# Kernel optimization log

Measured on AMD Instinct MI355X. Metric: run time of the kernel, lower is better.

## Reference

```python
import jax, jax.numpy as jnp
import numpy as np

N, E, D, H, C, G, L = 100000, 1600000, 128, 4, 32, 4096, 3  # nodes, edges, h_dim, heads, head_dim, graphs, conv blocks


def setup_inputs() -> dict:
    key = jax.random.key(0)
    ks = jax.random.split(key, 24)
    s = 0.05
    w = lambda k, shape: jax.random.normal(k, shape, jnp.float32) * s
    inp = {
        "x": jax.random.normal(ks[0], (N, D), jnp.float32),
        "edge_index": jax.random.randint(ks[1], (2, E), 0, N),
        "batch": jnp.sort(jax.random.randint(ks[2], (N,), 0, G)),
        # input TransformerConv (in=D, out=C per head, H heads, beta=True)
        "in_Wq": w(ks[3], (D, D)), "in_bq": jnp.zeros((D,), jnp.float32),
        "in_Wk": w(ks[4], (D, D)), "in_bk": jnp.zeros((D,), jnp.float32),
        "in_Wv": w(ks[5], (D, D)), "in_bv": jnp.zeros((D,), jnp.float32),
        "in_Ws": w(ks[6], (D, D)), "in_bs": jnp.zeros((D,), jnp.float32),
        "in_Wbeta": w(ks[7], (3 * D,)),
        # stacked conv blocks (L of them, in=out=D)
        "blk_Wq": w(ks[8], (L, D, D)), "blk_bq": jnp.zeros((L, D), jnp.float32),
        "blk_Wk": w(ks[9], (L, D, D)), "blk_bk": jnp.zeros((L, D), jnp.float32),
        "blk_Wv": w(ks[10], (L, D, D)), "blk_bv": jnp.zeros((L, D), jnp.float32),
        "blk_Ws": w(ks[11], (L, D, D)), "blk_bs": jnp.zeros((L, D), jnp.float32),
        "blk_Wbeta": w(ks[12], (L, 3 * D)),
        # MLP head
        "W1": w(ks[13], (D, 64)), "b1": jnp.zeros((64,), jnp.float32),
        "W2": w(ks[14], (64, 32)), "b2": jnp.zeros((32,), jnp.float32),
        "W3": w(ks[15], (32, 1)), "b3": jnp.zeros((1,), jnp.float32),
    }
    return inp


def transformer_conv(x, src, dst, Wq, bq, Wk, bk, Wv, bv, Ws, bs, Wbeta):
    # PyG TransformerConv, concat=True, root_weight=True, beta=True, eval mode
    q = (x @ Wq + bq).reshape(N, H, C)
    k = (x @ Wk + bk).reshape(N, H, C)
    v = (x @ Wv + bv).reshape(N, H, C)
    # per-edge attention logits: message j=src -> i=dst
    alpha = jnp.einsum("ehc,ehc->eh", q[dst], k[src]) / jnp.sqrt(jnp.float32(C))  # [E,H]
    m = jax.ops.segment_max(alpha, dst, num_segments=N)
    m = jnp.where(jnp.isfinite(m), m, 0.0)
    e = jnp.exp(alpha - m[dst])
    denom = jax.ops.segment_sum(e, dst, num_segments=N)
    a = e / (denom[dst] + 1e-16)  # segment softmax over in-edges of dst
    msg = a[..., None] * v[src]  # [E,H,C]
    out = jax.ops.segment_sum(msg, dst, num_segments=N).reshape(N, H * C)
    x_r = x @ Ws + bs
    beta = jax.nn.sigmoid(jnp.concatenate([out, x_r, out - x_r], axis=-1) @ Wbeta)[:, None]
    return beta * x_r + (1.0 - beta) * out


def reference(x, edge_index, batch, in_Wq, in_bq, in_Wk, in_bk, in_Wv, in_bv,
              in_Ws, in_bs, in_Wbeta, blk_Wq, blk_bq, blk_Wk, blk_bk, blk_Wv,
              blk_bv, blk_Ws, blk_bs, blk_Wbeta, W1, b1, W2, b2, W3, b3):
    src, dst = edge_index[0], edge_index[1]
    h = jax.nn.relu(transformer_conv(x, src, dst, in_Wq, in_bq, in_Wk, in_bk,
                                     in_Wv, in_bv, in_Ws, in_bs, in_Wbeta))
    for l in range(L):  # dropout is identity in eval mode
        h = jax.nn.relu(transformer_conv(h, src, dst, blk_Wq[l], blk_bq[l],
                                         blk_Wk[l], blk_bk[l], blk_Wv[l], blk_bv[l],
                                         blk_Ws[l], blk_bs[l], blk_Wbeta[l]))
    # global mean pool over graphs
    sums = jax.ops.segment_sum(h, batch, num_segments=G)
    cnt = jax.ops.segment_sum(jnp.ones((N, 1), h.dtype), batch, num_segments=G)
    g = sums / jnp.maximum(cnt, 1.0)
    g = jax.nn.relu(g @ W1 + b1)
    g = jax.nn.relu(g @ W2 + b2)
    return jax.nn.sigmoid(g @ W3 + b3)
```

## Files before the change

kernel.cpp:

```cpp
#include <hip/hip_runtime.h>
#include <hip/hip_bf16.h>
#include <cstdint>

#define DH 128
#define NB 256
#define NBK 1024

typedef __attribute__((ext_vector_type(8))) short short8;
typedef __attribute__((ext_vector_type(4))) float floatx4;
typedef __attribute__((ext_vector_type(2))) float floatx2;

__device__ __forceinline__ float bflo(unsigned u) { return __uint_as_float(u << 16); }
__device__ __forceinline__ float bfhi(unsigned u) { return __uint_as_float(u & 0xffff0000u); }

__device__ __forceinline__ unsigned pk_bf16(float a, float b) {
  return ((unsigned)__bfloat16_as_ushort(__float2bfloat16(b)) << 16)
       | (unsigned)__bfloat16_as_ushort(__float2bfloat16(a));
}

template<int CTRL>
__device__ __forceinline__ float dpp_add(float x) {
  int y = __builtin_amdgcn_update_dpp(0, __float_as_int(x), CTRL, 0xf, 0xf, true);
  return x + __int_as_float(y);
}


__global__ __launch_bounds__(256)
void csr_p1(const int* __restrict__ dst, int* __restrict__ hist, int E, int chunk) {
  __shared__ int cnt[NBK];
  const int blk = blockIdx.x, tid = threadIdx.x;
  for (int c = tid; c < NBK; c += 256) cnt[c] = 0;
  __syncthreads();
  int base = blk * chunk;
  int end = base + chunk; if (end > E) end = E;
  for (int e = base + tid; e < end; e += 256) atomicAdd(&cnt[dst[e] >> 7], 1);
  __syncthreads();
  for (int c = tid; c < NBK; c += 256) hist[c * NB + blk] = cnt[c];
}

__global__ __launch_bounds__(256)
void csr_p2(int* __restrict__ hist, int* __restrict__ total) {
  int b = blockIdx.x * 4 + (threadIdx.x >> 6);
  int lane = threadIdx.x & 63;
  int4 v = *(int4*)&hist[b * NB + lane * 4];
  int s0 = v.x;
  int s1 = s0 + v.y;
  int s2 = s1 + v.z;
  int s3 = s2 + v.w;
  int t = s3;
  for (int d = 1; d < 64; d <<= 1) {
    int y = __shfl_up(t, d);
    if (lane >= d) t += y;
  }
  int excl = t - s3;
  int4 o;
  o.x = excl; o.y = excl + s0; o.z = excl + s1; o.w = excl + s2;
  *(int4*)&hist[b * NB + lane * 4] = o;
  if (lane == 63) total[b] = t;
}

__global__ __launch_bounds__(1024)
void scan_tstart(const int* __restrict__ total, int* __restrict__ tstart) {
  __shared__ int sh[1024];
  int t = threadIdx.x;
  int v = total[t];
  sh[t] = v;
  __syncthreads();
  for (int d = 1; d < 1024; d <<= 1) {
    int x = (t >= d) ? sh[t - d] : 0;
    __syncthreads();
    sh[t] += x;
    __syncthreads();
  }
  tstart[t] = sh[t] - v;
}

__global__ __launch_bounds__(256)
void csr_p3(const int* __restrict__ src, const int* __restrict__ dst,
            const int* __restrict__ hist, const int* __restrict__ tstart,
            int* __restrict__ part, int E, int chunk) {
  __shared__ int cur[NBK];
  const int blk = blockIdx.x, tid = threadIdx.x;
  for (int c = tid; c < NBK; c += 256) cur[c] = hist[c * NB + blk] + tstart[c];
  __syncthreads();
  int base = blk * chunk;
  int end = base + chunk; if (end > E) end = E;
  for (int e = base + tid; e < end; e += 256) {
    int d = dst[e];
    int b = d >> 7;
    int pos = atomicAdd(&cur[b], 1);
    part[pos] = (src[e] << 7) | (d & 127);
  }
}

__global__ __launch_bounds__(256)
void csr_p4(const int* __restrict__ part, const int* __restrict__ tstart,
            const int* __restrict__ total, int* __restrict__ deg,
            int* __restrict__ off, int* __restrict__ csr, int Nn) {
  __shared__ int lcnt[128], lscan[128], lcur[128];
  const int b = blockIdx.x, tid = threadIdx.x;
  const int p0 = tstart[b];
  const int m = total[b];
  if (tid < 128) lcnt[tid] = 0;
  __syncthreads();
  for (int k = tid; k < m; k += 256) atomicAdd(&lcnt[part[p0 + k] & 127], 1);
  __syncthreads();
  if (tid < 128) lscan[tid] = lcnt[tid];
  __syncthreads();
  for (int d = 1; d < 128; d <<= 1) {
    int v = 0;
    if (tid < 128 && tid >= d) v = lscan[tid - d];
    __syncthreads();
    if (tid < 128) lscan[tid] += v;
    __syncthreads();
  }
  if (tid < 128) {
    int ex = lscan[tid] - lcnt[tid];
    lcur[tid] = ex;
    int n = (b << 7) + tid;
    if (n < Nn) { deg[n] = lcnt[tid]; off[n] = p0 + ex; }
  }
  __syncthreads();
  for (int k = tid; k < m; k += 256) {
    int pk = part[p0 + k];
    int pos = p0 + atomicAdd(&lcur[pk & 127], 1);
    csr[pos] = pk >> 7;
  }
}


__global__ void goff_kernel(const int* __restrict__ batch, int* __restrict__ goff,
                            int N, int G) {
  int g = blockIdx.x * 256 + threadIdx.x;
  if (g > G) return;
  if (g == G) { goff[G] = N; return; }
  int lo = 0, hi = N;
  while (lo < hi) { int mid = (lo + hi) >> 1; if (batch[mid] < g) lo = mid + 1; else hi = mid; }
  goff[g] = lo;
}


__global__ __launch_bounds__(256)
void pack_w_kernel(const float* __restrict__ iWq, const float* __restrict__ iWk,
                   const float* __restrict__ iWv, const float* __restrict__ iWs,
                   const float* __restrict__ ibq, const float* __restrict__ ibk,
                   const float* __restrict__ ibv, const float* __restrict__ ibs,
                   const float* __restrict__ bWq, const float* __restrict__ bWk,
                   const float* __restrict__ bWv, const float* __restrict__ bWs,
                   const float* __restrict__ bbq, const float* __restrict__ bbk,
                   const float* __restrict__ bbv, const float* __restrict__ bbs,
                   __hip_bfloat16* __restrict__ WT2, float* __restrict__ bcat) {
  const int layer = blockIdx.x / 65;
  const int bid = blockIdx.x % 65;
  const float *Wq, *Wk, *Wv, *Ws, *bq, *bk, *bv, *bs;
  if (layer == 0) {
    Wq = iWq; Wk = iWk; Wv = iWv; Ws = iWs; bq = ibq; bk = ibk; bv = ibv; bs = ibs;
  } else {
    int m = layer - 1;
    Wq = bWq + (size_t)m * DH * DH; Wk = bWk + (size_t)m * DH * DH;
    Wv = bWv + (size_t)m * DH * DH; Ws = bWs + (size_t)m * DH * DH;
    bq = bbq + (size_t)m * DH; bk = bbk + (size_t)m * DH;
    bv = bbv + (size_t)m * DH; bs = bbs + (size_t)m * DH;
  }
  unsigned short* WT2l = (unsigned short*)WT2 + (size_t)layer * 65536;
  float* bcl = bcat + layer * 512;

  if (bid == 64) {
    for (int c = threadIdx.x; c < 512; c += 256) {
      int which = c >> 7, cc = c & 127;
      const float* b = (which == 0) ? bq : (which == 1) ? bk : (which == 2) ? bv : bs;
      bcl[c] = b[cc];
    }
    return;
  }
  __shared__ float tile[32][33];
  const int which = bid >> 4, kb = (bid >> 2) & 3, cb = bid & 3;
  const float* W = (which == 0) ? Wq : (which == 1) ? Wk : (which == 2) ? Wv : Ws;
  const int tx = threadIdx.x & 31, ty = threadIdx.x >> 5;
#pragma unroll
  for (int r = ty; r < 32; r += 8)
    tile[r][tx] = W[(kb * 32 + r) * 128 + cb * 32 + tx];
  __syncthreads();
  const int t = threadIdx.x;
  const int mt_sel = t >> 7;
  const int s4 = (t & 127) * 4;
  const int l16 = s4 >> 5;
  const int quad = (s4 >> 3) & 3;
  const int j0 = s4 & 7;
  const int cl = mt_sel * 16 + l16;
  const int kr = quad * 8 + j0;
  float f0 = tile[kr + 0][cl];
  float f1 = tile[kr + 1][cl];
  float f2 = tile[kr + 2][cl];
  float f3 = tile[kr + 3][cl];
  const int mt = which * 8 + cb * 2 + mt_sel;
  const int o = mt * 2048 + kb * 512 + l16 * 32 + quad * 8 + j0;
  uint2 w;
  w.x = pk_bf16(f0, f1);
  w.y = pk_bf16(f2, f3);
  *(uint2*)&WT2l[o] = w;
}


template<int F32IN>
__global__ __launch_bounds__(256)
void gemm_qkvs(const void* __restrict__ Xin, const short* __restrict__ WT2,
               const float* __restrict__ bc,
               unsigned int* __restrict__ qout,
               unsigned int* __restrict__ kvp,
               unsigned int* __restrict__ xrout, int Nn) {
  __shared__ short As[32][132];
  const int row0 = blockIdx.x * 32;
  const int tid = threadIdx.x;

#pragma unroll
  for (int p = 0; p < 2; ++p) {
    int chunk = p * 256 + tid;
    int r = chunk >> 4, c8 = chunk & 15;
    int row = row0 + r; if (row >= Nn) row = Nn - 1;
    if (F32IN) {
      const float* xf = (const float*)Xin + (size_t)row * 128 + c8 * 8;
      float4 f0 = *(const float4*)xf;
      float4 f1 = *(const float4*)(xf + 4);
      int4 pk;
      ((unsigned*)&pk)[0] = pk_bf16(f0.x, f0.y);
      ((unsigned*)&pk)[1] = pk_bf16(f0.z, f0.w);
      ((unsigned*)&pk)[2] = pk_bf16(f1.x, f1.y);
      ((unsigned*)&pk)[3] = pk_bf16(f1.z, f1.w);
      *(int4*)&As[r][c8 * 8] = pk;
    } else {
      *(int4*)&As[r][c8 * 8] = *(const int4*)((const short*)Xin + (size_t)row * 128 + c8 * 8);
    }
  }
  __syncthreads();

  const int w = tid >> 6, lane = tid & 63, quad = lane >> 4, l16 = lane & 15;

  short8 xf[2][4];
#pragma unroll
  for (int nt = 0; nt < 2; ++nt)
#pragma unroll
    for (int kt = 0; kt < 4; ++kt)
      xf[nt][kt] = *(const short8*)&As[nt * 16 + l16][kt * 32 + quad * 8];

  const int fbase = l16 * 32 + quad * 8;

  if (w == 0 || w == 3) {
    unsigned int* outp = (w == 0) ? qout : xrout;
    const int mbase = (w == 0) ? 0 : 24;
#pragma unroll
    for (int i = 0; i < 8; ++i) {
      const int mt = mbase + i;
      short8 af[4];
#pragma unroll
      for (int kt = 0; kt < 4; ++kt)
        af[kt] = *(const short8*)&WT2[mt * 2048 + kt * 512 + fbase];
      float4 bias = *(const float4*)&bc[mt * 16 + quad * 4];
      const int wc = (i * 16 + quad * 4);
#pragma unroll
      for (int nt = 0; nt < 2; ++nt) {
        floatx4 acc = (floatx4){0.f, 0.f, 0.f, 0.f};
#pragma unroll
        for (int kt = 0; kt < 4; ++kt)
          acc = __builtin_amdgcn_mfma_f32_16x16x32_bf16(af[kt], xf[nt][kt], acc, 0, 0, 0);
        int node = row0 + nt * 16 + l16;
        if (node < Nn) {
          uint2 o;
          o.x = pk_bf16(acc[0] + bias.x, acc[1] + bias.y);
          o.y = pk_bf16(acc[2] + bias.z, acc[3] + bias.w);
          *(uint2*)&outp[(size_t)node * 64 + (wc >> 1)] = o;
        }
      }
    }
  } else {
    const int kb = 8 + (w - 1) * 4;
    const int vb = 16 + (w - 1) * 4;
#pragma unroll
    for (int i = 0; i < 4; ++i) {
      const int mk = kb + i, mv = vb + i;
      short8 afk[4], afv[4];
#pragma unroll
      for (int kt = 0; kt < 4; ++kt) {
        afk[kt] = *(const short8*)&WT2[mk * 2048 + kt * 512 + fbase];
        afv[kt] = *(const short8*)&WT2[mv * 2048 + kt * 512 + fbase];
      }
      float4 bk4 = *(const float4*)&bc[mk * 16 + quad * 4];
      float4 bv4 = *(const float4*)&bc[mv * 16 + quad * 4];
      const int krel = (w - 1) * 64 + i * 16 + quad * 4;
#pragma unroll
      for (int nt = 0; nt < 2; ++nt) {
        floatx4 ak = (floatx4){0.f, 0.f, 0.f, 0.f};
        floatx4 av = (floatx4){0.f, 0.f, 0.f, 0.f};
#pragma unroll
        for (int kt = 0; kt < 4; ++kt) {
          ak = __builtin_amdgcn_mfma_f32_16x16x32_bf16(afk[kt], xf[nt][kt], ak, 0, 0, 0);
          av = __builtin_amdgcn_mfma_f32_16x16x32_bf16(afv[kt], xf[nt][kt], av, 0, 0, 0);
        }
        int node = row0 + nt * 16 + l16;
        if (node < Nn) {
          int d0 = __builtin_amdgcn_cvt_pk_fp8_f32(ak[0] + bk4.x, ak[1] + bk4.y, 0, false);
          d0 = __builtin_amdgcn_cvt_pk_fp8_f32(av[0] + bv4.x, av[1] + bv4.y, d0, true);
          int d1 = __builtin_amdgcn_cvt_pk_fp8_f32(ak[2] + bk4.z, ak[3] + bk4.w, 0, false);
          d1 = __builtin_amdgcn_cvt_pk_fp8_f32(av[2] + bv4.z, av[3] + bv4.w, d1, true);
          uint2 o; o.x = (unsigned)d0; o.y = (unsigned)d1;
          *(uint2*)&kvp[(size_t)node * 64 + (krel >> 1)] = o;
        }
      }
    }
  }
}


__global__ __launch_bounds__(256)
void attn_kernel(unsigned int* __restrict__ q_h, const uint4* __restrict__ kvq,
                 const uint4* __restrict__ xr4, const int* __restrict__ off,
                 const int* __restrict__ deg, const int* __restrict__ csr,
                 const float* __restrict__ Wb, int Nn) {
  int wv = __builtin_amdgcn_readfirstlane(threadIdx.x >> 6);
  int i = blockIdx.x * 4 + wv;
  if (i >= Nn) return;
  const int l = threadIdx.x & 63;
  const int j = l & 15;
  const int g = l >> 4;

  const float QS = 0.17677669529663687f * 1.4426950408889634f;
  uint4 qw = ((const uint4*)q_h)[(size_t)i * 16 + j];
  float q0 = bflo(qw.x) * QS, q1 = bfhi(qw.x) * QS;
  float q2 = bflo(qw.y) * QS, q3 = bfhi(qw.y) * QS;
  float q4 = bflo(qw.z) * QS, q5 = bfhi(qw.z) * QS;
  float q6 = bflo(qw.w) * QS, q7 = bfhi(qw.w) * QS;

  const int e0 = off[i];
  const int dg = deg[i];
  const int eend = e0 + dg;

  float denA = 0.f, denB = 0.f;
  float aA[8] = {0.f, 0.f, 0.f, 0.f, 0.f, 0.f, 0.f, 0.f};
  float aB[8] = {0.f, 0.f, 0.f, 0.f, 0.f, 0.f, 0.f, 0.f};

  auto comp = [&](const uint4& kv, bool valid, float& den, float (&a)[8]) {
    floatx2 k0 = __builtin_amdgcn_cvt_pk_f32_fp8((int)kv.x, false);
    floatx2 v0 = __builtin_amdgcn_cvt_pk_f32_fp8((int)kv.x, true);
    floatx2 k1 = __builtin_amdgcn_cvt_pk_f32_fp8((int)kv.y, false);
    floatx2 v1 = __builtin_amdgcn_cvt_pk_f32_fp8((int)kv.y, true);
    floatx2 k2 = __builtin_amdgcn_cvt_pk_f32_fp8((int)kv.z, false);
    floatx2 v2 = __builtin_amdgcn_cvt_pk_f32_fp8((int)kv.z, true);
    floatx2 k3 = __builtin_amdgcn_cvt_pk_f32_fp8((int)kv.w, false);
    floatx2 v3 = __builtin_amdgcn_cvt_pk_f32_fp8((int)kv.w, true);
    float d = q0 * k0.x + q1 * k0.y + q2 * k1.x + q3 * k1.y
            + q4 * k2.x + q5 * k2.y + q6 * k3.x + q7 * k3.y;
    d = dpp_add<0xB1>(d);
    d = dpp_add<0x4E>(d);
    float p = valid ? exp2f(d) : 0.f;
    den += p;
    a[0] += p * v0.x; a[1] += p * v0.y; a[2] += p * v1.x; a[3] += p * v1.y;
    a[4] += p * v2.x; a[5] += p * v2.y; a[6] += p * v3.x; a[7] += p * v3.y;
  };

  for (int e = e0; e < eend; e += 64) {
    const int rem = eend - e;
    const int take = (rem < 64) ? rem : 64;
    int il = e + l; if (il >= eend) il = eend - 1;
    const int sv = csr[il];

    for (int b = 0; b < take; b += 16) {
      uint4 kv0, kv1, kv2, kv3;
      bool p0 = false, p1 = false, p2 = false, p3 = false;
      const int c0 = b + g, c1 = b + 4 + g, c2 = b + 8 + g, c3 = b + 12 + g;
      {
        p0 = c0 < take;
        int s = __shfl(sv, p0 ? c0 : 0);
        kv0 = kvq[(unsigned)((s << 4) | j)];
      }
      if (b + 4 < take) {
        p1 = c1 < take;
        int s = __shfl(sv, p1 ? c1 : 0);
        kv1 = kvq[(unsigned)((s << 4) | j)];
      }
      if (b + 8 < take) {
        p2 = c2 < take;
        int s = __shfl(sv, p2 ? c2 : 0);
        kv2 = kvq[(unsigned)((s << 4) | j)];
      }
      if (b + 12 < take) {
        p3 = c3 < take;
        int s = __shfl(sv, p3 ? c3 : 0);
        kv3 = kvq[(unsigned)((s << 4) | j)];
      }
      comp(kv0, p0, denA, aA);
      if (b + 4 < take)  comp(kv1, p1, denB, aB);
      if (b + 8 < take)  comp(kv2, p2, denA, aA);
      if (b + 12 < take) comp(kv3, p3, denB, aB);
    }
  }

  uint4 xw = xr4[(size_t)i * 16 + j];
  float4 wo0 = *(const float4*)&Wb[8 * j];
  float4 wo1 = *(const float4*)&Wb[8 * j + 4];
  float4 wx0 = *(const float4*)&Wb[128 + 8 * j];
  float4 wx1 = *(const float4*)&Wb[128 + 8 * j + 4];
  float4 wd0 = *(const float4*)&Wb[256 + 8 * j];
  float4 wd1 = *(const float4*)&Wb[256 + 8 * j + 4];

  float den = denA + denB;
  float a0 = aA[0] + aB[0], a1 = aA[1] + aB[1], a2 = aA[2] + aB[2], a3 = aA[3] + aB[3];
  float a4 = aA[4] + aB[4], a5 = aA[5] + aB[5], a6 = aA[6] + aB[6], a7 = aA[7] + aB[7];

  den += __shfl_xor(den, 16); den += __shfl_xor(den, 32);
  a0 += __shfl_xor(a0, 16); a0 += __shfl_xor(a0, 32);
  a1 += __shfl_xor(a1, 16); a1 += __shfl_xor(a1, 32);
  a2 += __shfl_xor(a2, 16); a2 += __shfl_xor(a2, 32);
  a3 += __shfl_xor(a3, 16); a3 += __shfl_xor(a3, 32);
  a4 += __shfl_xor(a4, 16); a4 += __shfl_xor(a4, 32);
  a5 += __shfl_xor(a5, 16); a5 += __shfl_xor(a5, 32);
  a6 += __shfl_xor(a6, 16); a6 += __shfl_xor(a6, 32);
  a7 += __shfl_xor(a7, 16); a7 += __shfl_xor(a7, 32);

  float inv = 1.f / (den + 1e-16f);
  float o0 = a0 * inv, o1 = a1 * inv, o2 = a2 * inv, o3 = a3 * inv;
  float o4 = a4 * inv, o5 = a5 * inv, o6 = a6 * inv, o7 = a7 * inv;

  float x0 = bflo(xw.x), x1 = bfhi(xw.x);
  float x2 = bflo(xw.y), x3 = bfhi(xw.y);
  float x4 = bflo(xw.z), x5 = bfhi(xw.z);
  float x6 = bflo(xw.w), x7 = bfhi(xw.w);

  float c = o0 * wo0.x + o1 * wo0.y + o2 * wo0.z + o3 * wo0.w
          + o4 * wo1.x + o5 * wo1.y + o6 * wo1.z + o7 * wo1.w
          + x0 * wx0.x + x1 * wx0.y + x2 * wx0.z + x3 * wx0.w
          + x4 * wx1.x + x5 * wx1.y + x6 * wx1.z + x7 * wx1.w
          + (o0 - x0) * wd0.x + (o1 - x1) * wd0.y + (o2 - x2) * wd0.z + (o3 - x3) * wd0.w
          + (o4 - x4) * wd1.x + (o5 - x5) * wd1.y + (o6 - x6) * wd1.z + (o7 - x7) * wd1.w;
  c = dpp_add<0xB1>(c);
  c = dpp_add<0x4E>(c);
  c = dpp_add<0x141>(c);
  c = dpp_add<0x140>(c);
  float beta = 1.f / (1.f + __expf(-c));

  if (g == 0) {
    float h0 = fmaxf(beta * x0 + (1.f - beta) * o0, 0.f);
    float h1 = fmaxf(beta * x1 + (1.f - beta) * o1, 0.f);
    float h2 = fmaxf(beta * x2 + (1.f - beta) * o2, 0.f);
    float h3 = fmaxf(beta * x3 + (1.f - beta) * o3, 0.f);
    float h4 = fmaxf(beta * x4 + (1.f - beta) * o4, 0.f);
    float h5 = fmaxf(beta * x5 + (1.f - beta) * o5, 0.f);
    float h6 = fmaxf(beta * x6 + (1.f - beta) * o6, 0.f);
    float h7 = fmaxf(beta * x7 + (1.f - beta) * o7, 0.f);
    uint4 hw;
    hw.x = pk_bf16(h0, h1);
    hw.y = pk_bf16(h2, h3);
    hw.z = pk_bf16(h4, h5);
    hw.w = pk_bf16(h6, h7);
    ((uint4*)q_h)[(size_t)i * 16 + j] = hw;
  }
}


__global__ __launch_bounds__(128)
void poolmlp_kernel(const unsigned short* __restrict__ h, const int* __restrict__ goff,
                    const float* __restrict__ W1, const float* __restrict__ b1,
                    const float* __restrict__ W2, const float* __restrict__ b2,
                    const float* __restrict__ W3, const float* __restrict__ b3,
                    float* __restrict__ out) {
  int g = blockIdx.x;
  int t = threadIdx.x;
  int n0 = goff[g], cnt = goff[g + 1] - n0;
  float s = 0.f;
  for (int n = n0; n < n0 + cnt; ++n) s += bflo(h[(size_t)n * 128 + t]);
  __shared__ float gv[128];
  __shared__ float t1[64];
  __shared__ float t2[32];
  gv[t] = s / fmaxf((float)cnt, 1.0f);
  __syncthreads();
  if (t < 64) {
    float a = b1[t];
    for (int k = 0; k < 128; ++k) a += gv[k] * W1[k * 64 + t];
    t1[t] = fmaxf(a, 0.f);
  }
  __syncthreads();
  if (t < 32) {
    float a = b2[t];
    for (int k = 0; k < 64; ++k) a += t1[k] * W2[k * 32 + t];
    t2[t] = fmaxf(a, 0.f);
  }
  __syncthreads();
  if (t == 0) {
    float a = b3[0];
    for (int k = 0; k < 32; ++k) a += t2[k] * W3[k];
    out[g] = 1.f / (1.f + __expf(-a));
  }
}


extern "C" void kernel_launch(void* const* d_in, const int* in_sizes, int n_in,
                              void* d_out, int out_size, void* d_ws, size_t ws_size,
                              hipStream_t stream) {
  const float* x = (const float*)d_in[0];
  const int* edge_index = (const int*)d_in[1];
  const int* batch = (const int*)d_in[2];
  const int N = in_sizes[0] / DH;
  const int E = in_sizes[1] / 2;
  const int G = out_size;
  const int* src = edge_index;
  const int* dst = edge_index + E;

  const float* in_Wq = (const float*)d_in[3];
  const float* in_bq = (const float*)d_in[4];
  const float* in_Wk = (const float*)d_in[5];
  const float* in_bk = (const float*)d_in[6];
  const float* in_Wv = (const float*)d_in[7];
  const float* in_bv = (const float*)d_in[8];
  const float* in_Ws = (const float*)d_in[9];
  const float* in_bs = (const float*)d_in[10];
  const float* in_Wbeta = (const float*)d_in[11];
  const float* blk_Wq = (const float*)d_in[12];
  const float* blk_bq = (const float*)d_in[13];
  const float* blk_Wk = (const float*)d_in[14];
  const float* blk_bk = (const float*)d_in[15];
  const float* blk_Wv = (const float*)d_in[16];
  const float* blk_bv = (const float*)d_in[17];
  const float* blk_Ws = (const float*)d_in[18];
  const float* blk_bs = (const float*)d_in[19];
  const float* blk_Wbeta = (const float*)d_in[20];

  char* p = (char*)d_ws;
  auto take = [&](size_t bytes) { char* r = p; p += (bytes + 255) & ~(size_t)255; return r; };
  __hip_bfloat16* h0 = (__hip_bfloat16*)take((size_t)N * DH * 2);
  __hip_bfloat16* h1 = (__hip_bfloat16*)take((size_t)N * DH * 2);
  unsigned char* kvp = (unsigned char*)take((size_t)N * 256);
  unsigned short* xr = (unsigned short*)take((size_t)N * DH * 2);
  __hip_bfloat16* WT2 = (__hip_bfloat16*)take((size_t)4 * 512 * DH * 2);
  float* bcat = (float*)take((size_t)4 * 512 * 4);
  int* deg    = (int*)take((size_t)N * 4);
  int* off    = (int*)take((size_t)N * 4);
  int* csr    = (int*)take((size_t)E * 4);
  int* part   = (int*)take((size_t)E * 4);
  int* hist   = (int*)take((size_t)NB * NBK * 4);
  int* total  = (int*)take(NBK * 4);
  int* tstart = (int*)take(NBK * 4);
  int* goff   = (int*)take((size_t)(G + 1) * 4);
  (void)n_in;
  if ((size_t)(p - (char*)d_ws) > ws_size) return;

  const int NBUCK = (N + 127) >> 7;
  const int chunk = (E + NB - 1) / NB;

  csr_p1<<<NB, 256, 0, stream>>>(dst, hist, E, chunk);
  csr_p2<<<NBK / 4, 256, 0, stream>>>(hist, total);
  scan_tstart<<<1, 1024, 0, stream>>>(total, tstart);
  csr_p3<<<NB, 256, 0, stream>>>(src, dst, hist, tstart, part, E, chunk);
  csr_p4<<<NBUCK, 256, 0, stream>>>(part, tstart, total, deg, off, csr, N);

  goff_kernel<<<(G + 256) / 256, 256, 0, stream>>>(batch, goff, N, G);

  pack_w_kernel<<<4 * 65, 256, 0, stream>>>(
      in_Wq, in_Wk, in_Wv, in_Ws, in_bq, in_bk, in_bv, in_bs,
      blk_Wq, blk_Wk, blk_Wv, blk_Ws, blk_bq, blk_bk, blk_bv, blk_bs,
      WT2, bcat);

  for (int l = 0; l < 4; ++l) {
    const float* Wb = (l == 0) ? in_Wbeta : blk_Wbeta + (size_t)(l - 1) * 3 * DH;
    const short* WT2l = (const short*)WT2 + (size_t)l * 65536;
    const float* bcl = bcat + (size_t)l * 512;
    __hip_bfloat16* hin  = (l & 1) ? h1 : h0;
    __hip_bfloat16* qbuf = (l & 1) ? h0 : h1;
    if (l == 0) {
      gemm_qkvs<1><<<(N + 31) / 32, 256, 0, stream>>>((const void*)x, WT2l, bcl,
          (unsigned int*)qbuf, (unsigned int*)kvp, (unsigned int*)xr, N);
    } else {
      gemm_qkvs<0><<<(N + 31) / 32, 256, 0, stream>>>((const void*)hin, WT2l, bcl,
          (unsigned int*)qbuf, (unsigned int*)kvp, (unsigned int*)xr, N);
    }
    attn_kernel<<<(N + 3) / 4, 256, 0, stream>>>((unsigned int*)qbuf, (const uint4*)kvp,
        (const uint4*)xr, off, deg, csr, Wb, N);
  }

  poolmlp_kernel<<<G, 128, 0, stream>>>((const unsigned short*)h0, goff,
      (const float*)d_in[21], (const float*)d_in[22],
      (const float*)d_in[23], (const float*)d_in[24],
      (const float*)d_in[25], (const float*)d_in[26],
      (float*)d_out);
}
```

Measured before the change: 678.2 us.

## Fuse CSR build, weight packing and first GEMM into fewer kernel launches

Independent preprocessing kernels (histogram pass, weight packing, graph offset search) are merged into one launch, and the CSR scatter pass is co-launched with the layer-0 QKVS GEMM in a single grid partitioned by block index. Offsets and degrees are packed into one int2 array, so attention reads one 8-byte value per node instead of two separate loads. The aim is to cut launch overhead and let independent work overlap on the GPU. In exchange, shared memory is sized for the largest branch, and the mixed-role kernels may see uneven block runtimes.

```diff
diff --git a/kernel.cpp b/kernel.cpp
--- a/kernel.cpp
+++ b/kernel.cpp
@@ -25,10 +25,8 @@
 }
 
 
-__global__ __launch_bounds__(256)
-void csr_p1(const int* __restrict__ dst, int* __restrict__ hist, int E, int chunk) {
-  __shared__ int cnt[NBK];
-  const int blk = blockIdx.x, tid = threadIdx.x;
+__device__ void csr_p1_body(int* cnt, const int* __restrict__ dst,
+                            int* __restrict__ hist, int E, int chunk, int blk, int tid) {
   for (int c = tid; c < NBK; c += 256) cnt[c] = 0;
   __syncthreads();
   int base = blk * chunk;
@@ -38,152 +36,31 @@
   for (int c = tid; c < NBK; c += 256) hist[c * NB + blk] = cnt[c];
 }
 
-__global__ __launch_bounds__(256)
-void csr_p2(int* __restrict__ hist, int* __restrict__ total) {
-  int b = blockIdx.x * 4 + (threadIdx.x >> 6);
-  int lane = threadIdx.x & 63;
-  int4 v = *(int4*)&hist[b * NB + lane * 4];
-  int s0 = v.x;
-  int s1 = s0 + v.y;
-  int s2 = s1 + v.z;
-  int s3 = s2 + v.w;
-  int t = s3;
-  for (int d = 1; d < 64; d <<= 1) {
-    int y = __shfl_up(t, d);
-    if (lane >= d) t += y;
-  }
-  int excl = t - s3;
-  int4 o;
-  o.x = excl; o.y = excl + s0; o.z = excl + s1; o.w = excl + s2;
-  *(int4*)&hist[b * NB + lane * 4] = o;
-  if (lane == 63) total[b] = t;
-}
-
-__global__ __launch_bounds__(1024)
-void scan_tstart(const int* __restrict__ total, int* __restrict__ tstart) {
-  __shared__ int sh[1024];
-  int t = threadIdx.x;
-  int v = total[t];
-  sh[t] = v;
-  __syncthreads();
-  for (int d = 1; d < 1024; d <<= 1) {
-    int x = (t >= d) ? sh[t - d] : 0;
-    __syncthreads();
-    sh[t] += x;
-    __syncthreads();
-  }
-  tstart[t] = sh[t] - v;
-}
-
-__global__ __launch_bounds__(256)
-void csr_p3(const int* __restrict__ src, const int* __restrict__ dst,
-            const int* __restrict__ hist, const int* __restrict__ tstart,
-            int* __restrict__ part, int E, int chunk) {
-  __shared__ int cur[NBK];
-  const int blk = blockIdx.x, tid = threadIdx.x;
-  for (int c = tid; c < NBK; c += 256) cur[c] = hist[c * NB + blk] + tstart[c];
-  __syncthreads();
-  int base = blk * chunk;
-  int end = base + chunk; if (end > E) end = E;
-  for (int e = base + tid; e < end; e += 256) {
-    int d = dst[e];
-    int b = d >> 7;
-    int pos = atomicAdd(&cur[b], 1);
-    part[pos] = (src[e] << 7) | (d & 127);
-  }
-}
-
-__global__ __launch_bounds__(256)
-void csr_p4(const int* __restrict__ part, const int* __restrict__ tstart,
-            const int* __restrict__ total, int* __restrict__ deg,
-            int* __restrict__ off, int* __restrict__ csr, int Nn) {
-  __shared__ int lcnt[128], lscan[128], lcur[128];
-  const int b = blockIdx.x, tid = threadIdx.x;
-  const int p0 = tstart[b];
-  const int m = total[b];
-  if (tid < 128) lcnt[tid] = 0;
-  __syncthreads();
-  for (int k = tid; k < m; k += 256) atomicAdd(&lcnt[part[p0 + k] & 127], 1);
-  __syncthreads();
-  if (tid < 128) lscan[tid] = lcnt[tid];
-  __syncthreads();
-  for (int d = 1; d < 128; d <<= 1) {
-    int v = 0;
-    if (tid < 128 && tid >= d) v = lscan[tid - d];
-    __syncthreads();
-    if (tid < 128) lscan[tid] += v;
-    __syncthreads();
-  }
-  if (tid < 128) {
-    int ex = lscan[tid] - lcnt[tid];
-    lcur[tid] = ex;
-    int n = (b << 7) + tid;
-    if (n < Nn) { deg[n] = lcnt[tid]; off[n] = p0 + ex; }
-  }
-  __syncthreads();
-  for (int k = tid; k < m; k += 256) {
-    int pk = part[p0 + k];
-    int pos = p0 + atomicAdd(&lcur[pk & 127], 1);
-    csr[pos] = pk >> 7;
-  }
-}
-
-
-__global__ void goff_kernel(const int* __restrict__ batch, int* __restrict__ goff,
-                            int N, int G) {
-  int g = blockIdx.x * 256 + threadIdx.x;
-  if (g > G) return;
-  if (g == G) { goff[G] = N; return; }
-  int lo = 0, hi = N;
-  while (lo < hi) { int mid = (lo + hi) >> 1; if (batch[mid] < g) lo = mid + 1; else hi = mid; }
-  goff[g] = lo;
-}
-
-
-__global__ __launch_bounds__(256)
-void pack_w_kernel(const float* __restrict__ iWq, const float* __restrict__ iWk,
-                   const float* __restrict__ iWv, const float* __restrict__ iWs,
-                   const float* __restrict__ ibq, const float* __restrict__ ibk,
-                   const float* __restrict__ ibv, const float* __restrict__ ibs,
-                   const float* __restrict__ bWq, const float* __restrict__ bWk,
-                   const float* __restrict__ bWv, const float* __restrict__ bWs,
-                   const float* __restrict__ bbq, const float* __restrict__ bbk,
-                   const float* __restrict__ bbv, const float* __restrict__ bbs,
-                   __hip_bfloat16* __restrict__ WT2, float* __restrict__ bcat) {
-  const int layer = blockIdx.x / 65;
-  const int bid = blockIdx.x % 65;
-  const float *Wq, *Wk, *Wv, *Ws, *bq, *bk, *bv, *bs;
-  if (layer == 0) {
-    Wq = iWq; Wk = iWk; Wv = iWv; Ws = iWs; bq = ibq; bk = ibk; bv = ibv; bs = ibs;
-  } else {
-    int m = layer - 1;
-    Wq = bWq + (size_t)m * DH * DH; Wk = bWk + (size_t)m * DH * DH;
-    Wv = bWv + (size_t)m * DH * DH; Ws = bWs + (size_t)m * DH * DH;
-    bq = bbq + (size_t)m * DH; bk = bbk + (size_t)m * DH;
-    bv = bbv + (size_t)m * DH; bs = bbs + (size_t)m * DH;
-  }
-  unsigned short* WT2l = (unsigned short*)WT2 + (size_t)layer * 65536;
-  float* bcl = bcat + layer * 512;
-
+__device__ void pack_w_body(float* tileraw,
+                            const float* __restrict__ Wq, const float* __restrict__ Wk,
+                            const float* __restrict__ Wv, const float* __restrict__ Ws,
+                            const float* __restrict__ bq, const float* __restrict__ bk,
+                            const float* __restrict__ bv, const float* __restrict__ bs,
+                            unsigned short* __restrict__ WT2l, float* __restrict__ bcl,
+                            int bid, int tid) {
   if (bid == 64) {
-    for (int c = threadIdx.x; c < 512; c += 256) {
+    for (int c = tid; c < 512; c += 256) {
       int which = c >> 7, cc = c & 127;
       const float* b = (which == 0) ? bq : (which == 1) ? bk : (which == 2) ? bv : bs;
       bcl[c] = b[cc];
     }
     return;
   }
-  __shared__ float tile[32][33];
+  float (*tile)[33] = (float(*)[33])tileraw;
   const int which = bid >> 4, kb = (bid >> 2) & 3, cb = bid & 3;
   const float* W = (which == 0) ? Wq : (which == 1) ? Wk : (which == 2) ? Wv : Ws;
-  const int tx = threadIdx.x & 31, ty = threadIdx.x >> 5;
+  const int tx = tid & 31, ty = tid >> 5;
 #pragma unroll
   for (int r = ty; r < 32; r += 8)
     tile[r][tx] = W[(kb * 32 + r) * 128 + cb * 32 + tx];
   __syncthreads();
-  const int t = threadIdx.x;
-  const int mt_sel = t >> 7;
-  const int s4 = (t & 127) * 4;
+  const int mt_sel = tid >> 7;
+  const int s4 = (tid & 127) * 4;
   const int l16 = s4 >> 5;
   const int quad = (s4 >> 3) & 3;
   const int j0 = s4 & 7;
@@ -201,18 +78,11 @@
   *(uint2*)&WT2l[o] = w;
 }
 
-
 template<int F32IN>
-__global__ __launch_bounds__(256)
-void gemm_qkvs(const void* __restrict__ Xin, const short* __restrict__ WT2,
-               const float* __restrict__ bc,
-               unsigned int* __restrict__ qout,
-               unsigned int* __restrict__ kvp,
-               unsigned int* __restrict__ xrout, int Nn) {
-  __shared__ short As[32][132];
-  const int row0 = blockIdx.x * 32;
-  const int tid = threadIdx.x;
-
+__device__ void gemm_body(short (*As)[132], const void* __restrict__ Xin,
+                          const short* __restrict__ WT2, const float* __restrict__ bc,
+                          unsigned int* __restrict__ qout, unsigned int* __restrict__ kvp,
+                          unsigned int* __restrict__ xrout, int Nn, int row0, int tid) {
 #pragma unroll
   for (int p = 0; p < 2; ++p) {
     int chunk = p * 256 + tid;
@@ -310,12 +180,168 @@
   }
 }
 
+__device__ void csr_p3_body(int* cur, const int* __restrict__ src, const int* __restrict__ dst,
+                            const int* __restrict__ hist, const int* __restrict__ tstart,
+                            int* __restrict__ part, int E, int chunk, int blk, int tid) {
+  for (int c = tid; c < NBK; c += 256) cur[c] = hist[c * NB + blk] + tstart[c];
+  __syncthreads();
+  int base = blk * chunk;
+  int end = base + chunk; if (end > E) end = E;
+  for (int e = base + tid; e < end; e += 256) {
+    int d = dst[e];
+    int b = d >> 7;
+    int pos = atomicAdd(&cur[b], 1);
+    part[pos] = (src[e] << 7) | (d & 127);
+  }
+}
+
+
+__global__ __launch_bounds__(256)
+void fused_pre(const int* __restrict__ dst, int* __restrict__ hist, int E, int chunk,
+               const int* __restrict__ batch, int* __restrict__ goff, int N, int G,
+               const float* __restrict__ iWq, const float* __restrict__ iWk,
+               const float* __restrict__ iWv, const float* __restrict__ iWs,
+               const float* __restrict__ ibq, const float* __restrict__ ibk,
+               const float* __restrict__ ibv, const float* __restrict__ ibs,
+               const float* __restrict__ bWq, const float* __restrict__ bWk,
+               const float* __restrict__ bWv, const float* __restrict__ bWs,
+               const float* __restrict__ bbq, const float* __restrict__ bbk,
+               const float* __restrict__ bbv, const float* __restrict__ bbs,
+               __hip_bfloat16* __restrict__ WT2, float* __restrict__ bcat) {
+  __shared__ int smem[1056];
+  const int bid = blockIdx.x, tid = threadIdx.x;
+  if (bid < NB) {
+    csr_p1_body(smem, dst, hist, E, chunk, bid, tid);
+  } else if (bid < NB + 260) {
+    const int pb = bid - NB;
+    const int layer = pb / 65, sub = pb % 65;
+    const float *Wq, *Wk, *Wv, *Ws, *bq, *bk, *bv, *bs;
+    if (layer == 0) {
+      Wq = iWq; Wk = iWk; Wv = iWv; Ws = iWs; bq = ibq; bk = ibk; bv = ibv; bs = ibs;
+    } else {
+      int m = layer - 1;
+      Wq = bWq + (size_t)m * DH * DH; Wk = bWk + (size_t)m * DH * DH;
+      Wv = bWv + (size_t)m * DH * DH; Ws = bWs + (size_t)m * DH * DH;
+      bq = bbq + (size_t)m * DH; bk = bbk + (size_t)m * DH;
+      bv = bbv + (size_t)m * DH; bs = bbs + (size_t)m * DH;
+    }
+    pack_w_body((float*)smem, Wq, Wk, Wv, Ws, bq, bk, bv, bs,
+                (unsigned short*)WT2 + (size_t)layer * 65536, bcat + layer * 512, sub, tid);
+  } else {
+    int g = (bid - NB - 260) * 256 + tid;
+    if (g > G) return;
+    if (g == G) { goff[G] = N; return; }
+    int lo = 0, hi = N;
+    while (lo < hi) { int mid = (lo + hi) >> 1; if (batch[mid] < g) lo = mid + 1; else hi = mid; }
+    goff[g] = lo;
+  }
+}
+
+__global__ __launch_bounds__(256)
+void csr_p2(int* __restrict__ hist, int* __restrict__ total) {
+  int b = blockIdx.x * 4 + (threadIdx.x >> 6);
+  int lane = threadIdx.x & 63;
+  int4 v = *(int4*)&hist[b * NB + lane * 4];
+  int s0 = v.x;
+  int s1 = s0 + v.y;
+  int s2 = s1 + v.z;
+  int s3 = s2 + v.w;
+  int t = s3;
+  for (int d = 1; d < 64; d <<= 1) {
+    int y = __shfl_up(t, d);
+    if (lane >= d) t += y;
+  }
+  int excl = t - s3;
+  int4 o;
+  o.x = excl; o.y = excl + s0; o.z = excl + s1; o.w = excl + s2;
+  *(int4*)&hist[b * NB + lane * 4] = o;
+  if (lane == 63) total[b] = t;
+}
+
+__global__ __launch_bounds__(1024)
+void scan_tstart(const int* __restrict__ total, int* __restrict__ tstart) {
+  __shared__ int sh[1024];
+  int t = threadIdx.x;
+  int v = total[t];
+  sh[t] = v;
+  __syncthreads();
+  for (int d = 1; d < 1024; d <<= 1) {
+    int x = (t >= d) ? sh[t - d] : 0;
+    __syncthreads();
+    sh[t] += x;
+    __syncthreads();
+  }
+  tstart[t] = sh[t] - v;
+}
+
+__global__ __launch_bounds__(256)
+void fused_g0p3(const void* __restrict__ Xin, const short* __restrict__ WT2,
+                const float* __restrict__ bc,
+                unsigned int* __restrict__ qout, unsigned int* __restrict__ kvp,
+                unsigned int* __restrict__ xrout, int Nn,
+                const int* __restrict__ src, const int* __restrict__ dst,
+                const int* __restrict__ hist, const int* __restrict__ tstart,
+                int* __restrict__ part, int E, int chunk) {
+  __shared__ int4 smem4[528];
+  const int tid = threadIdx.x;
+  if (blockIdx.x < NB) {
+    csr_p3_body((int*)smem4, src, dst, hist, tstart, part, E, chunk, blockIdx.x, tid);
+  } else {
+    gemm_body<1>((short(*)[132])smem4, Xin, WT2, bc, qout, kvp, xrout, Nn,
+                 (blockIdx.x - NB) * 32, tid);
+  }
+}
+
+__global__ __launch_bounds__(256)
+void csr_p4(const int* __restrict__ part, const int* __restrict__ tstart,
+            const int* __restrict__ total, int2* __restrict__ offdeg,
+            int* __restrict__ csr, int Nn) {
+  __shared__ int lcnt[128], lscan[128], lcur[128];
+  const int b = blockIdx.x, tid = threadIdx.x;
+  const int p0 = tstart[b];
+  const int m = total[b];
+  if (tid < 128) lcnt[tid] = 0;
+  __syncthreads();
+  for (int k = tid; k < m; k += 256) atomicAdd(&lcnt[part[p0 + k] & 127], 1);
+  __syncthreads();
+  if (tid < 128) lscan[tid] = lcnt[tid];
+  __syncthreads();
+  for (int d = 1; d < 128; d <<= 1) {
+    int v = 0;
+    if (tid < 128 && tid >= d) v = lscan[tid - d];
+    __syncthreads();
+    if (tid < 128) lscan[tid] += v;
+    __syncthreads();
+  }
+  if (tid < 128) {
+    int ex = lscan[tid] - lcnt[tid];
+    lcur[tid] = ex;
+    int n = (b << 7) + tid;
+    if (n < Nn) offdeg[n] = make_int2(p0 + ex, lcnt[tid]);
+  }
+  __syncthreads();
+  for (int k = tid; k < m; k += 256) {
+    int pk = part[p0 + k];
+    int pos = p0 + atomicAdd(&lcur[pk & 127], 1);
+    csr[pos] = pk >> 7;
+  }
+}
+
+__global__ __launch_bounds__(256)
+void gemm_qkvs(const short* __restrict__ Xin, const short* __restrict__ WT2,
+               const float* __restrict__ bc,
+               unsigned int* __restrict__ qout, unsigned int* __restrict__ kvp,
+               unsigned int* __restrict__ xrout, int Nn) {
+  __shared__ int4 smem4[528];
+  gemm_body<0>((short(*)[132])smem4, (const void*)Xin, WT2, bc, qout, kvp, xrout, Nn,
+               blockIdx.x * 32, threadIdx.x);
+}
+
 
 __global__ __launch_bounds__(256)
 void attn_kernel(unsigned int* __restrict__ q_h, const uint4* __restrict__ kvq,
-                 const uint4* __restrict__ xr4, const int* __restrict__ off,
-                 const int* __restrict__ deg, const int* __restrict__ csr,
-                 const float* __restrict__ Wb, int Nn) {
+                 const uint4* __restrict__ xr4, const int2* __restrict__ offdeg,
+                 const int* __restrict__ csr, const float* __restrict__ Wb, int Nn) {
   int wv = __builtin_amdgcn_readfirstlane(threadIdx.x >> 6);
   int i = blockIdx.x * 4 + wv;
   if (i >= Nn) return;
@@ -325,13 +351,14 @@
 
   const float QS = 0.17677669529663687f * 1.4426950408889634f;
   uint4 qw = ((const uint4*)q_h)[(size_t)i * 16 + j];
+  int2 od = offdeg[i];
   float q0 = bflo(qw.x) * QS, q1 = bfhi(qw.x) * QS;
   float q2 = bflo(qw.y) * QS, q3 = bfhi(qw.y) * QS;
   float q4 = bflo(qw.z) * QS, q5 = bfhi(qw.z) * QS;
   float q6 = bflo(qw.w) * QS, q7 = bfhi(qw.w) * QS;
 
-  const int e0 = off[i];
-  const int dg = deg[i];
+  const int e0 = od.x;
+  const int dg = od.y;
   const int eend = e0 + dg;
 
   float denA = 0.f, denB = 0.f;
@@ -531,8 +558,7 @@
   unsigned short* xr = (unsigned short*)take((size_t)N * DH * 2);
   __hip_bfloat16* WT2 = (__hip_bfloat16*)take((size_t)4 * 512 * DH * 2);
   float* bcat = (float*)take((size_t)4 * 512 * 4);
-  int* deg    = (int*)take((size_t)N * 4);
-  int* off    = (int*)take((size_t)N * 4);
+  int2* offdeg = (int2*)take((size_t)N * 8);
   int* csr    = (int*)take((size_t)E * 4);
   int* part   = (int*)take((size_t)E * 4);
   int* hist   = (int*)take((size_t)NB * NBK * 4);
@@ -544,35 +570,37 @@
 
   const int NBUCK = (N + 127) >> 7;
   const int chunk = (E + NB - 1) / NB;
-
-  csr_p1<<<NB, 256, 0, stream>>>(dst, hist, E, chunk);
-  csr_p2<<<NBK / 4, 256, 0, stream>>>(hist, total);
-  scan_tstart<<<1, 1024, 0, stream>>>(total, tstart);
-  csr_p3<<<NB, 256, 0, stream>>>(src, dst, hist, tstart, part, E, chunk);
-  csr_p4<<<NBUCK, 256, 0, stream>>>(part, tstart, total, deg, off, csr, N);
-
-  goff_kernel<<<(G + 256) / 256, 256, 0, stream>>>(batch, goff, N, G);
-
-  pack_w_kernel<<<4 * 65, 256, 0, stream>>>(
+  const int gblocks = (G + 256) / 256;
+
+  fused_pre<<<NB + 260 + gblocks, 256, 0, stream>>>(
+      dst, hist, E, chunk, batch, goff, N, G,
       in_Wq, in_Wk, in_Wv, in_Ws, in_bq, in_bk, in_bv, in_bs,
       blk_Wq, blk_Wk, blk_Wv, blk_Ws, blk_bq, blk_bk, blk_bv, blk_bs,
       WT2, bcat);
 
-  for (int l = 0; l < 4; ++l) {
-    const float* Wb = (l == 0) ? in_Wbeta : blk_Wbeta + (size_t)(l - 1) * 3 * DH;
+  csr_p2<<<NBK / 4, 256, 0, stream>>>(hist, total);
+  scan_tstart<<<1, 1024, 0, stream>>>(total, tstart);
+
+  fused_g0p3<<<NB + (N + 31) / 32, 256, 0, stream>>>(
+      (const void*)x, (const short*)WT2, bcat,
+      (unsigned int*)h1, (unsigned int*)kvp, (unsigned int*)xr, N,
+      src, dst, hist, tstart, part, E, chunk);
+
+  csr_p4<<<NBUCK, 256, 0, stream>>>(part, tstart, total, offdeg, csr, N);
+
+  attn_kernel<<<(N + 3) / 4, 256, 0, stream>>>((unsigned int*)h1, (const uint4*)kvp,
+      (const uint4*)xr, offdeg, csr, in_Wbeta, N);
+
+  for (int l = 1; l < 4; ++l) {
+    const float* Wb = blk_Wbeta + (size_t)(l - 1) * 3 * DH;
     const short* WT2l = (const short*)WT2 + (size_t)l * 65536;
     const float* bcl = bcat + (size_t)l * 512;
     __hip_bfloat16* hin  = (l & 1) ? h1 : h0;
     __hip_bfloat16* qbuf = (l & 1) ? h0 : h1;
-    if (l == 0) {
-      gemm_qkvs<1><<<(N + 31) / 32, 256, 0, stream>>>((const void*)x, WT2l, bcl,
-          (unsigned int*)qbuf, (unsigned int*)kvp, (unsigned int*)xr, N);
-    } else {
-      gemm_qkvs<0><<<(N + 31) / 32, 256, 0, stream>>>((const void*)hin, WT2l, bcl,
-          (unsigned int*)qbuf, (unsigned int*)kvp, (unsigned int*)xr, N);
-    }
+    gemm_qkvs<<<(N + 31) / 32, 256, 0, stream>>>((const short*)hin, WT2l, bcl,
+        (unsigned int*)qbuf, (unsigned int*)kvp, (unsigned int*)xr, N);
     attn_kernel<<<(N + 3) / 4, 256, 0, stream>>>((unsigned int*)qbuf, (const uint4*)kvp,
-        (const uint4*)xr, off, deg, csr, Wb, N);
+        (const uint4*)xr, offdeg, csr, Wb, N);
   }
 
   poolmlp_kernel<<<G, 128, 0, stream>>>((const unsigned short*)h0, goff,
```

New measurement: 658.5 us. 2.9% less time.
